# Kernel optimization log

Measured on AMD Instinct MI355X. Metric: run time of the kernel, lower is better.

The kernel has to match this reference:

```python
import jax, jax.numpy as jnp
import numpy as np

B, O, T, C_IN, IMG, P, D = 16, 3, 8, 3, 224, 16, 768
HF = IMG // P  # 14x14 conv feature grid
S = 7          # ObjectsCrops output size (SxS per object per frame)


def setup_inputs() -> dict:
    key = jax.random.key(0)
    ks = jax.random.split(key, 6)
    x = jax.random.normal(ks[0], (B, C_IN, T, IMG, IMG), dtype=jnp.float32)
    # metadata: [B, O, T, 4] boxes (x1,y1,x2,y2) in pixel coords within [0,224]
    u = jax.random.uniform(ks[1], (B, O, T, 4), dtype=jnp.float32)
    bx1 = u[..., 0] * 160.0
    by1 = u[..., 1] * 160.0
    bw = 16.0 + u[..., 2] * 48.0
    bh = 16.0 + u[..., 3] * 48.0
    metadata = jnp.stack([bx1, by1, jnp.minimum(bx1 + bw, 224.0), jnp.minimum(by1 + bh, 224.0)], axis=-1)
    proj_w = jax.random.normal(ks[2], (D, C_IN, P, P), dtype=jnp.float32) * 0.02  # Conv3d kernel, tubelet dim (=1) squeezed
    proj_b = jnp.zeros((D,), dtype=jnp.float32)
    box_categories = jax.random.normal(ks[3], (T, O, D), dtype=jnp.float32) * 0.02
    w1 = jax.random.normal(ks[4], (4, D // 2), dtype=jnp.float32) * 0.1   # Linear(4, 384, bias=False)
    w2 = jax.random.normal(ks[5], (D // 2, D), dtype=jnp.float32) * 0.05  # Linear(384, 768, bias=False)
    return dict(x=x, metadata=metadata, proj_w=proj_w, proj_b=proj_b, box_categories=box_categories, w1=w1, w2=w2)


def _roi_crop(feat, boxes):
    # feat: [BT, C, Hf, Wf]; boxes: [BT, O, 4] (x1,y1,x2,y2) in feature-map coords
    BT, C, Hf, Wf = feat.shape
    x1, y1, x2, y2 = (boxes[..., i] for i in range(4))
    cell = (jnp.arange(S, dtype=feat.dtype) + 0.5) / S               # sample cell centers
    ys = y1[..., None] + cell * (y2 - y1)[..., None]                 # [BT,O,S]
    xs = x1[..., None] + cell * (x2 - x1)[..., None]
    yg = jnp.broadcast_to(ys[:, :, :, None], (BT, O, S, S)) - 0.5    # pixel centers at idx+0.5
    xg = jnp.broadcast_to(xs[:, :, None, :], (BT, O, S, S)) - 0.5
    y0f = jnp.floor(yg); x0f = jnp.floor(xg)
    wy = yg - y0f; wx = xg - x0f
    y0 = jnp.clip(y0f.astype(jnp.int32), 0, Hf - 1); y1i = jnp.clip(y0 + 1, 0, Hf - 1)
    x0 = jnp.clip(x0f.astype(jnp.int32), 0, Wf - 1); x1i = jnp.clip(x0 + 1, 0, Wf - 1)
    gather = jax.vmap(lambda fm, yy, xx: fm[:, yy, xx])              # [C,Hf,Wf],[O,S,S] -> [C,O,S,S]
    v00 = gather(feat, y0, x0); v01 = gather(feat, y0, x1i)
    v10 = gather(feat, y1i, x0); v11 = gather(feat, y1i, x1i)
    wy = wy[:, None]; wx = wx[:, None]                               # [BT,1,O,S,S]
    return (v00 * (1 - wy) * (1 - wx) + v01 * (1 - wy) * wx
            + v10 * wy * (1 - wx) + v11 * wy * wx)                   # [BT,C,O,S,S]


def reference(x, metadata, proj_w, proj_b, box_categories, w1, w2):
    Bs = x.shape[0]
    boxes = jnp.transpose(metadata, (0, 2, 1, 3))                    # [B,T,O,4] pixel coords
    # coordinate MLP on normalized boxes + per-(frame,object) category embedding
    box_emb = jax.nn.relu(jax.nn.relu((boxes / 224.0) @ w1) @ w2)    # [B,T,O,D]
    box_emb = box_categories[None] + box_emb
    # Conv3d patch embed: tubelet=1, stride==kernel -> non-overlapping patchify + GEMM
    xp = x.reshape(Bs, C_IN, T, HF, P, HF, P)
    feat = jnp.einsum('bcthpwq,dcpq->btdhw', xp, proj_w) + proj_b[None, None, :, None, None]
    feat = feat.reshape(Bs * T, D, HF, HF)
    fboxes = boxes.reshape(Bs * T, O, 4) * (HF / 224.0)              # boxes in feature coords
    crops = _roi_crop(feat, fboxes).reshape(Bs, T, D, O, S, S)
    xo = jnp.transpose(crops, (0, 3, 2, 1, 4, 5))                    # [B,O,C,T,S,S]
    emb = jnp.transpose(box_emb, (0, 2, 3, 1))                       # [B,O,D,T]
    xo = xo + emb[..., None, None]
    xo = xo.reshape(Bs * O, D, T, S * S)                             # flatten(3) on [N*O,C,T,H,W]
    return jnp.transpose(xo, (0, 2, 3, 1))                           # [B*O, T, S*S, D]
```

## Files before the change

### kernel.cpp

```cpp
#include <hip/hip_runtime.h>
#include <hip/hip_bf16.h>

typedef unsigned int u32;
typedef unsigned short ushort_t;
typedef __bf16 bf16x8 __attribute__((ext_vector_type(8)));
typedef float f32x4 __attribute__((ext_vector_type(4)));
typedef unsigned short ushort8 __attribute__((ext_vector_type(8)));
typedef unsigned short ushort4v __attribute__((ext_vector_type(4)));

#define GM 25088
#define GK 768
#define GN 768

__device__ __forceinline__ ushort_t f2bf(float f) {
    u32 u = __float_as_uint(f);
    u32 r = (u + 0x7FFFu + ((u >> 16) & 1u)) >> 16;
    return (ushort_t)r;
}

__device__ __forceinline__ f32x4 bf2f4(ushort4v u) {
    f32x4 f;
    #pragma unroll
    for (int e = 0; e < 4; ++e) f[e] = __uint_as_float(((u32)u[e]) << 16);
    return f;
}

__device__ __forceinline__ void load_lds16(const void* g, void* l) {
    __builtin_amdgcn_global_load_lds(
        (const __attribute__((address_space(1))) u32*)g,
        (__attribute__((address_space(3))) u32*)l, 16, 0, 0);
}

__global__ __launch_bounds__(256) void prep(const float* __restrict__ x,
                                            const float* __restrict__ projw,
                                            const float* __restrict__ meta,
                                            const float* __restrict__ w1,
                                            const float* __restrict__ w2,
                                            const float* __restrict__ cats,
                                            ushort_t* __restrict__ Ap,
                                            ushort_t* __restrict__ Wp,
                                            float* __restrict__ emb) {
    __shared__ float H[3][384];
    int bid = blockIdx.x;
    int tid = threadIdx.x;
    if (bid < 1176) {
        int g = bid * 256 + tid;
        int m = g / 12;
        int piece = g % 12;
        int w = m % 14, h = (m / 14) % 14, t = (m / 196) % 8, b = m / 1568;
        int c = piece >> 2, p0 = (piece & 3) * 4;
        const float* src = x + ((size_t)((b * 3 + c) * 8 + t) * 224 + h * 16 + p0) * 224 + w * 16;
        int xo = (m & 7) << 4;
        ushort_t* dst = Ap + (size_t)m * 768 + piece * 64;
        #pragma unroll
        for (int i = 0; i < 4; ++i) {
            const float* s = src + i * 224;
            f32x4 f0 = *(const f32x4*)(s);
            f32x4 f1 = *(const f32x4*)(s + 4);
            f32x4 f2 = *(const f32x4*)(s + 8);
            f32x4 f3 = *(const f32x4*)(s + 12);
            ushort8 r0, r1;
            r0[0] = f2bf(f0[0]); r0[1] = f2bf(f0[1]); r0[2] = f2bf(f0[2]); r0[3] = f2bf(f0[3]);
            r0[4] = f2bf(f1[0]); r0[5] = f2bf(f1[1]); r0[6] = f2bf(f1[2]); r0[7] = f2bf(f1[3]);
            r1[0] = f2bf(f2[0]); r1[1] = f2bf(f2[1]); r1[2] = f2bf(f2[2]); r1[3] = f2bf(f2[3]);
            r1[4] = f2bf(f3[0]); r1[5] = f2bf(f3[1]); r1[6] = f2bf(f3[2]); r1[7] = f2bf(f3[3]);
            int b0 = (i * 32) ^ xo;
            int b1 = (i * 32 + 16) ^ xo;
            *(ushort8*)(dst + (b0 >> 1)) = r0;
            *(ushort8*)(dst + (b1 >> 1)) = r1;
        }
    } else if (bid < 1212) {
        int g = (bid - 1176) * 256 + tid;
        int n = g / 12;
        int piece = g % 12;
        const float* src = projw + (size_t)n * 768 + piece * 64;
        int xo = (n & 7) << 4;
        ushort_t* dst = Wp + (size_t)n * 768 + piece * 64;
        #pragma unroll
        for (int i = 0; i < 4; ++i) {
            const float* s = src + i * 16;
            f32x4 f0 = *(const f32x4*)(s);
            f32x4 f1 = *(const f32x4*)(s + 4);
            f32x4 f2 = *(const f32x4*)(s + 8);
            f32x4 f3 = *(const f32x4*)(s + 12);
            ushort8 r0, r1;
            r0[0] = f2bf(f0[0]); r0[1] = f2bf(f0[1]); r0[2] = f2bf(f0[2]); r0[3] = f2bf(f0[3]);
            r0[4] = f2bf(f1[0]); r0[5] = f2bf(f1[1]); r0[6] = f2bf(f1[2]); r0[7] = f2bf(f1[3]);
            r1[0] = f2bf(f2[0]); r1[1] = f2bf(f2[1]); r1[2] = f2bf(f2[2]); r1[3] = f2bf(f2[3]);
            r1[4] = f2bf(f3[0]); r1[5] = f2bf(f3[1]); r1[6] = f2bf(f3[2]); r1[7] = f2bf(f3[3]);
            int b0 = (i * 32) ^ xo;
            int b1 = (i * 32 + 16) ^ xo;
            *(ushort8*)(dst + (b0 >> 1)) = r0;
            *(ushort8*)(dst + (b1 >> 1)) = r1;
        }
    } else {
        int bb = bid - 1212;
        int bt = bb / 3;
        int dc = bb % 3;
        int b = bt / 8, t = bt % 8;
        for (int idx = tid; idx < 3 * 384; idx += 256) {
            int o = idx / 384, j = idx % 384;
            const float* mp = meta + ((b * 3 + o) * 8 + t) * 4;
            float s = 0.f;
            #pragma unroll
            for (int i = 0; i < 4; ++i) s += (mp[i] * (1.0f / 224.0f)) * w1[i * 384 + j];
            H[o][j] = fmaxf(s, 0.f);
        }
        __syncthreads();
        int d = dc * 256 + tid;
        float acc[3] = {0.f, 0.f, 0.f};
        #pragma unroll 4
        for (int j = 0; j < 384; ++j) {
            float wv = w2[j * 768 + d];
            acc[0] += H[0][j] * wv;
            acc[1] += H[1][j] * wv;
            acc[2] += H[2][j] * wv;
        }
        #pragma unroll
        for (int o = 0; o < 3; ++o) {
            emb[((size_t)bt * 3 + o) * 768 + d] =
                fmaxf(acc[o], 0.f) + cats[(t * 3 + o) * 768 + d];
        }
    }
}

__global__ __launch_bounds__(256) void gemm_bt(const ushort_t* __restrict__ A,
                                               const ushort_t* __restrict__ Bt,
                                               const float* __restrict__ pb,
                                               ushort_t* __restrict__ Cb) {
    __shared__ ushort_t lA[2][128 * 64];
    __shared__ ushort_t lB[2][128 * 64];
    int tid = threadIdx.x;
    int bid = blockIdx.x;
    int wid = (bid & 7) * 147 + (bid >> 3);
    int bm = wid / 6;
    int bn = wid % 6;
    size_t m0 = (size_t)bm * 128, n0 = (size_t)bn * 128;
    int w = tid >> 6, lane = tid & 63;
    int wr = w >> 1, wc = w & 1;
    int r15 = lane & 15;
    int xoU = (lane & 7) << 3;

    f32x4 acc[4][4] = {};

    #define STAGE(buf, kt_)                                                        \
        {                                                                          \
            int k0_ = (kt_) * 64;                                                  \
            _Pragma("unroll")                                                      \
            for (int r = 0; r < 4; ++r) {                                          \
                int cidx = r * 256 + tid;                                          \
                int row = cidx >> 3;                                               \
                int col = (cidx & 7) * 8;                                          \
                load_lds16(A + ((m0 + row) * 768 + k0_ + col), &lA[buf][cidx * 8]);\
            }                                                                      \
            _Pragma("unroll")                                                      \
            for (int r = 0; r < 4; ++r) {                                          \
                int cidx = r * 256 + tid;                                          \
                int row = cidx >> 3;                                               \
                int col = (cidx & 7) * 8;                                          \
                load_lds16(Bt + ((n0 + row) * 768 + k0_ + col), &lB[buf][cidx * 8]);\
            }                                                                      \
        }

    STAGE(0, 0);
    __syncthreads();

    for (int kt = 0; kt < 12; ++kt) {
        int cur = kt & 1;
        if (kt < 11) STAGE(cur ^ 1, kt + 1);
        #pragma unroll
        for (int kk = 0; kk < 2; ++kk) {
            int cs = (kk * 32 + (lane >> 4) * 8) ^ xoU;
            bf16x8 af[4], bfr[4];
            #pragma unroll
            for (int mi = 0; mi < 4; ++mi)
                af[mi] = *(const bf16x8*)&lA[cur][(wr * 64 + mi * 16 + r15) * 64 + cs];
            #pragma unroll
            for (int ni = 0; ni < 4; ++ni)
                bfr[ni] = *(const bf16x8*)&lB[cur][(wc * 64 + ni * 16 + r15) * 64 + cs];
            #pragma unroll
            for (int mi = 0; mi < 4; ++mi)
                #pragma unroll
                for (int ni = 0; ni < 4; ++ni)
                    acc[mi][ni] = __builtin_amdgcn_mfma_f32_16x16x32_bf16(
                        af[mi], bfr[ni], acc[mi][ni], 0, 0, 0);
        }
        __syncthreads();
    }
    #undef STAGE

    int rbase = (lane >> 4) * 4;
    #pragma unroll
    for (int ni = 0; ni < 4; ++ni) {
        size_t col = n0 + wc * 64 + ni * 16 + r15;
        float pbv = pb[col];
        #pragma unroll
        for (int mi = 0; mi < 4; ++mi) {
            size_t row = m0 + wr * 64 + mi * 16 + rbase;
            #pragma unroll
            for (int j = 0; j < 4; ++j) {
                Cb[(row + j) * 768 + col] = f2bf(acc[mi][ni][j] + pbv);
            }
        }
    }
}

__global__ __launch_bounds__(192) void roi_kernel(const float* __restrict__ meta,
                                                  const ushort_t* __restrict__ featB,
                                                  const float* __restrict__ emb,
                                                  float* __restrict__ out) {
    int xcd = blockIdx.x & 7;
    int idx = blockIdx.x >> 3;
    int d = threadIdx.x * 4;

    for (int wi = idx; wi < 336; wi += 96) {
        int wid = xcd * 336 + wi;
        int i = wid % 7; int r = wid / 7;
        int o = r % 3; r /= 3;
        int t = r % 8;
        int b = r / 8;

        const float* mp = meta + ((b * 3 + o) * 8 + t) * 4;
        float x1 = mp[0] * (1.f / 16.f);
        float y1 = mp[1] * (1.f / 16.f);
        float x2 = mp[2] * (1.f / 16.f);
        float y2 = mp[3] * (1.f / 16.f);

        float ci = (i + 0.5f) * (1.f / 7.f);
        float yg = y1 + ci * (y2 - y1) - 0.5f;
        float y0f = floorf(yg);
        float wy = yg - y0f;
        int y0 = min(max((int)y0f, 0), 13);
        int y1c = min(y0 + 1, 13);

        int bt = b * 8 + t;
        const ushort_t* fbase = featB + (size_t)bt * 196 * 768;
        const float* ep = emb + ((size_t)bt * 3 + o) * 768;
        f32x4 ev = *(const f32x4*)(ep + d);

        #pragma unroll
        for (int j = 0; j < 7; ++j) {
            float cj = (j + 0.5f) * (1.f / 7.f);
            float xgv = x1 + cj * (x2 - x1) - 0.5f;
            float x0f = floorf(xgv);
            float wx = xgv - x0f;
            int x0 = min(max((int)x0f, 0), 13);
            int x1i = min(x0 + 1, 13);

            f32x4 v00 = bf2f4(*(const ushort4v*)(fbase + ((size_t)y0 * 14 + x0) * 768 + d));
            f32x4 v01 = bf2f4(*(const ushort4v*)(fbase + ((size_t)y0 * 14 + x1i) * 768 + d));
            f32x4 v10 = bf2f4(*(const ushort4v*)(fbase + ((size_t)y1c * 14 + x0) * 768 + d));
            f32x4 v11 = bf2f4(*(const ushort4v*)(fbase + ((size_t)y1c * 14 + x1i) * 768 + d));

            float w00 = (1.f - wy) * (1.f - wx);
            float w01 = (1.f - wy) * wx;
            float w10 = wy * (1.f - wx);
            float w11 = wy * wx;

            f32x4 rr;
            #pragma unroll
            for (int e = 0; e < 4; ++e)
                rr[e] = v00[e] * w00 + v01[e] * w01 + v10[e] * w10 + v11[e] * w11 + ev[e];

            int pp = i * 7 + j;
            *(f32x4*)(out + ((((size_t)(b * 3 + o) * 8 + t) * 49 + pp) * 768 + d)) = rr;
        }
    }
}

extern "C" void kernel_launch(void* const* d_in, const int* in_sizes, int n_in,
                              void* d_out, int out_size, void* d_ws, size_t ws_size,
                              hipStream_t stream) {
    const float* x     = (const float*)d_in[0];
    const float* meta  = (const float*)d_in[1];
    const float* projw = (const float*)d_in[2];
    const float* projb = (const float*)d_in[3];
    const float* cats  = (const float*)d_in[4];
    const float* w1    = (const float*)d_in[5];
    const float* w2    = (const float*)d_in[6];
    float* out = (float*)d_out;

    char* ws = (char*)d_ws;
    const size_t szA  = (size_t)GM * GK * 2;
    const size_t szW  = (size_t)GN * GK * 2;
    const size_t szFB = (size_t)GM * GN * 2;
    ushort_t* Ap    = (ushort_t*)(ws);
    ushort_t* Wp    = (ushort_t*)(ws + szA);
    ushort_t* featB = (ushort_t*)(ws + szA + szW);
    float*    emb   = (float*)(ws + szA + szW + szFB);

    prep<<<1596, 256, 0, stream>>>(x, projw, meta, w1, w2, cats, Ap, Wp, emb);
    gemm_bt<<<1176, 256, 0, stream>>>(Ap, Wp, projb, featB);
    roi_kernel<<<768, 192, 0, stream>>>(meta, featB, emb, out);
}
```

Baseline: 245.5 us.

## Stage patchify through LDS for coalesced image reads; one ROI row per block

The patchify step in prep now has one block per (b,t,h) strip. The block reads full 224-wide image rows in coalesced 32-byte chunks, converts them to bf16 into shared memory, and then writes the swizzled GEMM A rows from shared memory. This replaces the earlier per-patch strided 64-byte reads. The ROI kernel drops its grid-stride loop and launches one block per (b,o,t,row) work item, which raises parallelism at the cost of more blocks and an extra LDS round trip with a barrier in prep.

Measured after the change: 243.9 us. About the same (-0.6%).

```diff
diff --git a/kernel.cpp b/kernel.cpp
--- a/kernel.cpp
+++ b/kernel.cpp
@@ -23,6 +23,13 @@
     #pragma unroll
     for (int e = 0; e < 4; ++e) f[e] = __uint_as_float(((u32)u[e]) << 16);
     return f;
+}
+
+__device__ __forceinline__ ushort8 cvt8(f32x4 f0, f32x4 f1) {
+    ushort8 r;
+    r[0] = f2bf(f0[0]); r[1] = f2bf(f0[1]); r[2] = f2bf(f0[2]); r[3] = f2bf(f0[3]);
+    r[4] = f2bf(f1[0]); r[5] = f2bf(f1[1]); r[6] = f2bf(f1[2]); r[7] = f2bf(f1[3]);
+    return r;
 }
 
 __device__ __forceinline__ void load_lds16(const void* g, void* l) {
@@ -40,37 +47,40 @@
                                             ushort_t* __restrict__ Ap,
                                             ushort_t* __restrict__ Wp,
                                             float* __restrict__ emb) {
+    __shared__ ushort_t Lsm[3 * 16 * 232];
     __shared__ float H[3][384];
     int bid = blockIdx.x;
     int tid = threadIdx.x;
-    if (bid < 1176) {
-        int g = bid * 256 + tid;
-        int m = g / 12;
-        int piece = g % 12;
-        int w = m % 14, h = (m / 14) % 14, t = (m / 196) % 8, b = m / 1568;
-        int c = piece >> 2, p0 = (piece & 3) * 4;
-        const float* src = x + ((size_t)((b * 3 + c) * 8 + t) * 224 + h * 16 + p0) * 224 + w * 16;
-        int xo = (m & 7) << 4;
-        ushort_t* dst = Ap + (size_t)m * 768 + piece * 64;
-        #pragma unroll
-        for (int i = 0; i < 4; ++i) {
-            const float* s = src + i * 224;
-            f32x4 f0 = *(const f32x4*)(s);
+    if (bid < 1792) {
+        int h = bid % 14;
+        int t = (bid / 14) % 8;
+        int b = bid / 112;
+        for (int chunk = tid; chunk < 1344; chunk += 256) {
+            int c = chunk / 448;
+            int cc = chunk % 448;
+            int p = cc / 28;
+            int col0 = (cc % 28) * 8;
+            const float* s = x + ((size_t)((b * 3 + c) * 8 + t) * 224 + h * 16 + p) * 224 + col0;
+            f32x4 f0 = *(const f32x4*)s;
             f32x4 f1 = *(const f32x4*)(s + 4);
-            f32x4 f2 = *(const f32x4*)(s + 8);
-            f32x4 f3 = *(const f32x4*)(s + 12);
-            ushort8 r0, r1;
-            r0[0] = f2bf(f0[0]); r0[1] = f2bf(f0[1]); r0[2] = f2bf(f0[2]); r0[3] = f2bf(f0[3]);
-            r0[4] = f2bf(f1[0]); r0[5] = f2bf(f1[1]); r0[6] = f2bf(f1[2]); r0[7] = f2bf(f1[3]);
-            r1[0] = f2bf(f2[0]); r1[1] = f2bf(f2[1]); r1[2] = f2bf(f2[2]); r1[3] = f2bf(f2[3]);
-            r1[4] = f2bf(f3[0]); r1[5] = f2bf(f3[1]); r1[6] = f2bf(f3[2]); r1[7] = f2bf(f3[3]);
-            int b0 = (i * 32) ^ xo;
-            int b1 = (i * 32 + 16) ^ xo;
-            *(ushort8*)(dst + (b0 >> 1)) = r0;
-            *(ushort8*)(dst + (b1 >> 1)) = r1;
-        }
-    } else if (bid < 1212) {
-        int g = (bid - 1176) * 256 + tid;
+            *(ushort8*)&Lsm[(c * 16 + p) * 232 + col0] = cvt8(f0, f1);
+        }
+        __syncthreads();
+        int mbase = ((b * 8 + t) * 14 + h) * 14;
+        for (int chunk = tid; chunk < 1344; chunk += 256) {
+            int w = chunk / 96;
+            int kc = chunk % 96;
+            int k0 = kc * 8;
+            int c = k0 >> 8;
+            int p = (k0 >> 4) & 15;
+            int q0 = k0 & 15;
+            ushort8 r = *(const ushort8*)&Lsm[(c * 16 + p) * 232 + w * 16 + q0];
+            int mm = mbase + w;
+            int bytesw = (kc * 16) ^ ((mm & 7) << 4);
+            *(ushort8*)(Ap + (size_t)mm * 768 + (bytesw >> 1)) = r;
+        }
+    } else if (bid < 1828) {
+        int g = (bid - 1792) * 256 + tid;
         int n = g / 12;
         int piece = g % 12;
         const float* src = projw + (size_t)n * 768 + piece * 64;
@@ -83,18 +93,13 @@
             f32x4 f1 = *(const f32x4*)(s + 4);
             f32x4 f2 = *(const f32x4*)(s + 8);
             f32x4 f3 = *(const f32x4*)(s + 12);
-            ushort8 r0, r1;
-            r0[0] = f2bf(f0[0]); r0[1] = f2bf(f0[1]); r0[2] = f2bf(f0[2]); r0[3] = f2bf(f0[3]);
-            r0[4] = f2bf(f1[0]); r0[5] = f2bf(f1[1]); r0[6] = f2bf(f1[2]); r0[7] = f2bf(f1[3]);
-            r1[0] = f2bf(f2[0]); r1[1] = f2bf(f2[1]); r1[2] = f2bf(f2[2]); r1[3] = f2bf(f2[3]);
-            r1[4] = f2bf(f3[0]); r1[5] = f2bf(f3[1]); r1[6] = f2bf(f3[2]); r1[7] = f2bf(f3[3]);
             int b0 = (i * 32) ^ xo;
             int b1 = (i * 32 + 16) ^ xo;
-            *(ushort8*)(dst + (b0 >> 1)) = r0;
-            *(ushort8*)(dst + (b1 >> 1)) = r1;
+            *(ushort8*)(dst + (b0 >> 1)) = cvt8(f0, f1);
+            *(ushort8*)(dst + (b1 >> 1)) = cvt8(f2, f3);
         }
     } else {
-        int bb = bid - 1212;
+        int bb = bid - 1828;
         int bt = bb / 3;
         int dc = bb % 3;
         int b = bt / 8, t = bt % 8;
@@ -209,62 +214,58 @@
                                                   const ushort_t* __restrict__ featB,
                                                   const float* __restrict__ emb,
                                                   float* __restrict__ out) {
-    int xcd = blockIdx.x & 7;
-    int idx = blockIdx.x >> 3;
+    int bid = blockIdx.x;
+    int wid = (bid & 7) * 336 + (bid >> 3);
+    int i = wid % 7; int r = wid / 7;
+    int o = r % 3; r /= 3;
+    int t = r % 8;
+    int b = r / 8;
     int d = threadIdx.x * 4;
 
-    for (int wi = idx; wi < 336; wi += 96) {
-        int wid = xcd * 336 + wi;
-        int i = wid % 7; int r = wid / 7;
-        int o = r % 3; r /= 3;
-        int t = r % 8;
-        int b = r / 8;
-
-        const float* mp = meta + ((b * 3 + o) * 8 + t) * 4;
-        float x1 = mp[0] * (1.f / 16.f);
-        float y1 = mp[1] * (1.f / 16.f);
-        float x2 = mp[2] * (1.f / 16.f);
-        float y2 = mp[3] * (1.f / 16.f);
-
-        float ci = (i + 0.5f) * (1.f / 7.f);
-        float yg = y1 + ci * (y2 - y1) - 0.5f;
-        float y0f = floorf(yg);
-        float wy = yg - y0f;
-        int y0 = min(max((int)y0f, 0), 13);
-        int y1c = min(y0 + 1, 13);
-
-        int bt = b * 8 + t;
-        const ushort_t* fbase = featB + (size_t)bt * 196 * 768;
-        const float* ep = emb + ((size_t)bt * 3 + o) * 768;
-        f32x4 ev = *(const f32x4*)(ep + d);
-
-        #pragma unroll
-        for (int j = 0; j < 7; ++j) {
-            float cj = (j + 0.5f) * (1.f / 7.f);
-            float xgv = x1 + cj * (x2 - x1) - 0.5f;
-            float x0f = floorf(xgv);
-            float wx = xgv - x0f;
-            int x0 = min(max((int)x0f, 0), 13);
-            int x1i = min(x0 + 1, 13);
-
-            f32x4 v00 = bf2f4(*(const ushort4v*)(fbase + ((size_t)y0 * 14 + x0) * 768 + d));
-            f32x4 v01 = bf2f4(*(const ushort4v*)(fbase + ((size_t)y0 * 14 + x1i) * 768 + d));
-            f32x4 v10 = bf2f4(*(const ushort4v*)(fbase + ((size_t)y1c * 14 + x0) * 768 + d));
-            f32x4 v11 = bf2f4(*(const ushort4v*)(fbase + ((size_t)y1c * 14 + x1i) * 768 + d));
-
-            float w00 = (1.f - wy) * (1.f - wx);
-            float w01 = (1.f - wy) * wx;
-            float w10 = wy * (1.f - wx);
-            float w11 = wy * wx;
-
-            f32x4 rr;
-            #pragma unroll
-            for (int e = 0; e < 4; ++e)
-                rr[e] = v00[e] * w00 + v01[e] * w01 + v10[e] * w10 + v11[e] * w11 + ev[e];
-
-            int pp = i * 7 + j;
-            *(f32x4*)(out + ((((size_t)(b * 3 + o) * 8 + t) * 49 + pp) * 768 + d)) = rr;
-        }
+    const float* mp = meta + ((b * 3 + o) * 8 + t) * 4;
+    float x1 = mp[0] * (1.f / 16.f);
+    float y1 = mp[1] * (1.f / 16.f);
+    float x2 = mp[2] * (1.f / 16.f);
+    float y2 = mp[3] * (1.f / 16.f);
+
+    float ci = (i + 0.5f) * (1.f / 7.f);
+    float yg = y1 + ci * (y2 - y1) - 0.5f;
+    float y0f = floorf(yg);
+    float wy = yg - y0f;
+    int y0 = min(max((int)y0f, 0), 13);
+    int y1c = min(y0 + 1, 13);
+
+    int bt = b * 8 + t;
+    const ushort_t* fbase = featB + (size_t)bt * 196 * 768;
+    const float* ep = emb + ((size_t)bt * 3 + o) * 768;
+    f32x4 ev = *(const f32x4*)(ep + d);
+
+    #pragma unroll
+    for (int j = 0; j < 7; ++j) {
+        float cj = (j + 0.5f) * (1.f / 7.f);
+        float xgv = x1 + cj * (x2 - x1) - 0.5f;
+        float x0f = floorf(xgv);
+        float wx = xgv - x0f;
+        int x0 = min(max((int)x0f, 0), 13);
+        int x1i = min(x0 + 1, 13);
+
+        f32x4 v00 = bf2f4(*(const ushort4v*)(fbase + ((size_t)y0 * 14 + x0) * 768 + d));
+        f32x4 v01 = bf2f4(*(const ushort4v*)(fbase + ((size_t)y0 * 14 + x1i) * 768 + d));
+        f32x4 v10 = bf2f4(*(const ushort4v*)(fbase + ((size_t)y1c * 14 + x0) * 768 + d));
+        f32x4 v11 = bf2f4(*(const ushort4v*)(fbase + ((size_t)y1c * 14 + x1i) * 768 + d));
+
+        float w00 = (1.f - wy) * (1.f - wx);
+        float w01 = (1.f - wy) * wx;
+        float w10 = wy * (1.f - wx);
+        float w11 = wy * wx;
+
+        f32x4 rr;
+        #pragma unroll
+        for (int e = 0; e < 4; ++e)
+            rr[e] = v00[e] * w00 + v01[e] * w01 + v10[e] * w10 + v11[e] * w11 + ev[e];
+
+        int pp = i * 7 + j;
+        *(f32x4*)(out + ((((size_t)(b * 3 + o) * 8 + t) * 49 + pp) * 768 + d)) = rr;
     }
 }
 
@@ -289,7 +290,7 @@
     ushort_t* featB = (ushort_t*)(ws + szA + szW);
     float*    emb   = (float*)(ws + szA + szW + szFB);
 
-    prep<<<1596, 256, 0, stream>>>(x, projw, meta, w1, w2, cats, Ap, Wp, emb);
+    prep<<<2212, 256, 0, stream>>>(x, projw, meta, w1, w2, cats, Ap, Wp, emb);
     gemm_bt<<<1176, 256, 0, stream>>>(Ap, Wp, projb, featB);
-    roi_kernel<<<768, 192, 0, stream>>>(meta, featB, emb, out);
-}
+    roi_kernel<<<2688, 192, 0, stream>>>(meta, featB, emb, out);
+}
```
